# Kernel tuning notes

Measured on AMD Instinct MI355X. Metric: run time of the kernel, lower is better.

The kernel has to match this reference:

```python
import jax, jax.numpy as jnp
from jax import lax
import numpy as np

IMG = 2048.0            # square image size (W=H)
STRIDES = [32, 64, 128]
FEATS = [64, 32, 16]    # IMG / stride
NUM_CLASSES = 80
BATCH = 8
SCORE_THRESH = 0.2
NMS_THRESH = 0.6
TOPK = 1000             # topk_candidates per level
DETS = 100              # detections_per_img


def make_anchors(fs, stride):
    # square anchors of size==stride centered on the feature grid (AnchorGenerator with ratio 1.0)
    c = (jnp.arange(fs, dtype=jnp.float32) + 0.5) * stride
    cy, cx = jnp.meshgrid(c, c, indexing='ij')
    cx, cy = cx.reshape(-1), cy.reshape(-1)
    h = stride / 2.0
    return jnp.stack([cx - h, cy - h, cx + h, cy + h], axis=1)


def setup_inputs() -> dict:
    key = jax.random.key(0)
    inp = {}
    for i, (fs, s) in enumerate(zip(FEATS, STRIDES)):
        hw = fs * fs
        key, k1, k2, k3 = jax.random.split(key, 4)
        inp[f'cls{i}'] = jax.random.normal(k1, (BATCH, hw, NUM_CLASSES), jnp.float32)
        inp[f'reg{i}'] = jax.random.uniform(k2, (BATCH, hw, 4), jnp.float32)
        inp[f'ctr{i}'] = jax.random.normal(k3, (BATCH, hw), jnp.float32)
        inp[f'anc{i}'] = make_anchors(fs, float(s))
    return inp


def _decode(rel, boxes):
    # BoxLinearCoder.decode_single with normalize_by_size=True
    cx = 0.5 * (boxes[:, 0] + boxes[:, 2])
    cy = 0.5 * (boxes[:, 1] + boxes[:, 3])
    w = boxes[:, 2] - boxes[:, 0]
    h = boxes[:, 3] - boxes[:, 1]
    rel = rel * jnp.stack([w, h, w, h], axis=1)
    return jnp.stack([cx - rel[:, 0], cy - rel[:, 1], cx + rel[:, 2], cy + rel[:, 3]], axis=1)


def _iou(b):
    # torchvision box_iou on a single set of boxes [N,4] -> [N,N]
    area = (b[:, 2] - b[:, 0]) * (b[:, 3] - b[:, 1])
    lt = jnp.maximum(b[:, None, :2], b[None, :, :2])
    rb = jnp.minimum(b[:, None, 2:], b[None, :, 2:])
    wh = jnp.clip(rb - lt, 0.0)
    inter = wh[..., 0] * wh[..., 1]
    return inter / (area[:, None] + area[None, :] - inter)


def _greedy_keep(iou):
    # classic greedy NMS on score-sorted boxes: suppress j>i with iou>thresh if i kept
    n = iou.shape[0]
    idx = jnp.arange(n)
    def body(i, keep):
        supp = keep[i] & (iou[i] > NMS_THRESH) & (idx > i)
        return keep & ~supp
    return lax.fori_loop(0, n, body, jnp.ones((n,), bool))


def _per_image(cls_l, reg_l, ctr_l, anc_l):
    boxes, scores, labels = [], [], []
    for cls, reg, ctr, anc in zip(cls_l, reg_l, ctr_l, anc_l):
        hw, c = cls.shape
        # scores = sqrt(sigmoid(cls) * sigmoid(ctrness)) flattened over anchors*classes
        sc = jnp.sqrt(jax.nn.sigmoid(cls) * jax.nn.sigmoid(ctr)[:, None]).reshape(-1)
        sc = jnp.where(sc > SCORE_THRESH, sc, -1.0)  # score threshold as mask (static shapes)
        ts, ti = lax.top_k(sc, TOPK)                 # per-level top-k candidates
        aidx = ti // c
        lab = ti % c
        b = jnp.clip(_decode(reg[aidx], anc[aidx]), 0.0, IMG)  # decode + clip to image
        boxes.append(b); scores.append(ts); labels.append(lab)
    boxes = jnp.concatenate(boxes)    # [3*TOPK, 4]
    scores = jnp.concatenate(scores)  # [3*TOPK]
    labels = jnp.concatenate(labels)  # [3*TOPK]
    n = scores.shape[0]
    # batched_nms via per-class coordinate offsets
    off = labels.astype(boxes.dtype) * (IMG + 1.0)
    ss, oi = lax.top_k(scores, n)     # sort candidates by score desc
    bs = boxes[oi] + off[oi][:, None]
    keep = lax.stop_gradient(_greedy_keep(_iou(bs)))
    fsc = jnp.where(keep & (ss > 0), ss, -1.0)
    fs, fi = lax.top_k(fsc, DETS)     # keep detections_per_img; score==-1 marks padding
    return boxes[oi][fi], fs, labels[oi][fi]


def reference(cls0, cls1, cls2, reg0, reg1, reg2, ctr0, ctr1, ctr2, anc0, anc1, anc2):
    f = jax.vmap(lambda c0, c1, c2, r0, r1, r2, t0, t1, t2: _per_image(
        [c0, c1, c2], [r0, r1, r2], [t0, t1, t2], [anc0, anc1, anc2]))
    return f(cls0, cls1, cls2, reg0, reg1, reg2, ctr0, ctr1, ctr2)
```

## Files before the change

### kernel.cpp

```cpp
#include <hip/hip_runtime.h>

#define NCLS  80
#define SELK  256
#define NLVL  3
#define NIMG  8
#define DETS  100
#define CAP   512
#define NDEC  512
#define HBINS 4096
#define NHBLK 16
#define NCBLK 16
#define QBASE 0x3F800000u
#define QMAX  0x41C80000u
#define IMGSZ 2048.0f


__device__ __forceinline__ float sigm(float x) {
    if (x >= 0.f) return 1.f / (1.f + expf(-x));
    float e = expf(x);
    return e / (1.f + e);
}

__device__ __forceinline__ unsigned int qbits(float ea, float t1) {
    return __float_as_uint(__fmul_rn(__fadd_rn(1.f, ea), t1));
}

__device__ __forceinline__ void lvl_select(int level,
    const float* c0, const float* c1, const float* c2,
    const float* t0, const float* t1, const float* t2,
    const float** cls, const float** ctr, int* hw) {
    if (level == 0)      { *cls = c0; *ctr = t0; *hw = 4096; }
    else if (level == 1) { *cls = c1; *ctr = t1; *hw = 1024; }
    else                 { *cls = c2; *ctr = t2; *hw = 256; }
}


__global__ void k_hist(const float* c0, const float* c1, const float* c2,
                       const float* t0, const float* t1, const float* t2,
                       unsigned int* parts, unsigned int* counters) {
    int level = blockIdx.z, img = blockIdx.y;
    int pair = img * NLVL + level;
    if (blockIdx.x == 0 && threadIdx.x == 0) counters[pair * 16] = 0;
    const float* cls; const float* ctr; int hw;
    lvl_select(level, c0, c1, c2, t0, t1, t2, &cls, &ctr, &hw);
    int n4 = hw * (NCLS / 4);
    const float4* cl4 = (const float4*)(cls + (size_t)img * hw * NCLS);
    const float* ct = ctr + (size_t)img * hw;
    __shared__ unsigned int h[HBINS];
    for (int i = threadIdx.x; i < HBINS; i += 256) h[i] = 0;
    __syncthreads();
    for (int i = blockIdx.x * 256 + threadIdx.x; i < n4; i += NHBLK * 256) {
        float4 v = cl4[i];
        int a = i / (NCLS / 4);
        float eb = expf(-ct[a]);
        float t1 = __fadd_rn(1.f, eb);
        #pragma unroll
        for (int k = 0; k < 4; ++k) {
            float x = (k == 0) ? v.x : (k == 1) ? v.y : (k == 2) ? v.z : v.w;
            unsigned int qb = qbits(expf(-x), t1);
            if (qb < QMAX) {
                unsigned int bin = (qb - QBASE) >> 13;
                if (bin > HBINS - 1) bin = HBINS - 1;
                atomicAdd(&h[bin], 1u);
            }
        }
    }
    __syncthreads();
    unsigned int* P = parts + ((size_t)(pair * NHBLK + blockIdx.x)) * HBINS;
    for (int i = threadIdx.x; i < HBINS; i += 256) P[i] = h[i];
}


__global__ void k_collect(const float* c0, const float* c1, const float* c2,
                          const float* t0, const float* t1, const float* t2,
                          const unsigned int* parts, unsigned int* counters,
                          unsigned long long* buf) {
    int level = blockIdx.z, img = blockIdx.y;
    int pair = img * NLVL + level;
    int tid = threadIdx.x;
    __shared__ unsigned int hb[HBINS];
    __shared__ unsigned int segsum[256];
    __shared__ unsigned int pref[256];
    __shared__ unsigned long long sbuf[CAP];
    __shared__ unsigned int scnt, sbase, Vsh;
    if (tid == 0) scnt = 0;
    {
        unsigned int acc[HBINS / 256];
        #pragma unroll
        for (int j = 0; j < HBINS / 256; ++j) acc[j] = 0;
        for (int blk = 0; blk < NHBLK; ++blk) {
            const unsigned int* P = parts + ((size_t)(pair * NHBLK + blk)) * HBINS;
            #pragma unroll
            for (int j = 0; j < HBINS / 256; ++j) acc[j] += P[tid + 256 * j];
        }
        #pragma unroll
        for (int j = 0; j < HBINS / 256; ++j) hb[tid + 256 * j] = acc[j];
    }
    __syncthreads();
    {
        unsigned int seg = 0;
        #pragma unroll
        for (int j = 0; j < 16; ++j) seg += hb[16 * tid + j];
        segsum[tid] = seg;
        pref[tid] = seg;
        __syncthreads();
        for (int off = 1; off < 256; off <<= 1) {
            unsigned int v = (tid >= off) ? pref[tid - off] : 0u;
            __syncthreads();
            pref[tid] += v;
            __syncthreads();
        }
        unsigned int incl = pref[tid];
        unsigned int excl = incl - segsum[tid];
        if (excl < (unsigned int)SELK && incl >= (unsigned int)SELK) {
            unsigned int cum = excl; int B = HBINS - 1;
            for (int b = 16 * tid; b < 16 * tid + 16; ++b) {
                cum += hb[b];
                if (cum >= (unsigned int)SELK) { B = b; break; }
            }
            Vsh = (B >= HBINS - 1) ? QMAX : (QBASE + ((unsigned int)(B + 1) << 13));
        }
        if (tid == 255 && pref[255] < (unsigned int)SELK)
            Vsh = QMAX;
    }
    __syncthreads();
    unsigned int V = Vsh;

    const float* cls; const float* ctr; int hw;
    lvl_select(level, c0, c1, c2, t0, t1, t2, &cls, &ctr, &hw);
    int n4 = hw * (NCLS / 4);
    const float4* cl4 = (const float4*)(cls + (size_t)img * hw * NCLS);
    const float* ct = ctr + (size_t)img * hw;
    for (int i = blockIdx.x * 256 + tid; i < n4; i += NCBLK * 256) {
        float4 v = cl4[i];
        int a = i / (NCLS / 4);
        float cta = ct[a];
        float eb = expf(-cta);
        float t1 = __fadd_rn(1.f, eb);
        #pragma unroll
        for (int k = 0; k < 4; ++k) {
            float x = (k == 0) ? v.x : (k == 1) ? v.y : (k == 2) ? v.z : v.w;
            unsigned int qb = qbits(expf(-x), t1);
            if (qb < V) {
                float s = sqrtf(sigm(x) * sigm(cta));
                unsigned int e = (unsigned int)(4 * i + k);
                unsigned int p = ((unsigned int)level << 19) | e;
                unsigned int slot = atomicAdd(&scnt, 1u);
                if (slot < CAP)
                    sbuf[slot] = ((unsigned long long)__float_as_uint(s) << 32) | (~p);
            }
        }
    }
    __syncthreads();
    unsigned int cl_n = scnt; if (cl_n > CAP) cl_n = CAP;
    if (tid == 0)
        sbase = atomicAdd(&counters[pair * 16], cl_n);
    __syncthreads();
    unsigned int base = sbase;
    for (unsigned int idx = tid; idx < cl_n; idx += 256) {
        unsigned int g = base + idx;
        if (g < CAP) buf[(size_t)pair * CAP + g] = sbuf[idx];
    }
}


__global__ void __launch_bounds__(512)
k_merge_nms(const unsigned long long* buf, const unsigned int* counters,
            const float* r0, const float* r1, const float* r2,
            const float* a0, const float* a1, const float* a2,
            float* out) {
    int img = blockIdx.x;
    int tid = threadIdx.x;
    __shared__ unsigned long long S[3 * CAP];
    __shared__ unsigned long long Mbuf[2 * CAP];
    __shared__ float4 sbx[64]; __shared__ float sar[64];
    __shared__ float4 koff[DETS]; __shared__ float karr[DETS];
    __shared__ float4 kb[DETS]; __shared__ float ks[DETS]; __shared__ int kl[DETS];
    __shared__ float4 rb[DETS]; __shared__ int rl[DETS];
    float4* wbox = (float4*)Mbuf;
    int*    wlab = (int*)(S + CAP);

    for (int l = 0; l < NLVL; ++l) {
        int pair = img * NLVL + l;
        int c = (int)counters[pair * 16]; if (c > CAP) c = CAP;
        const unsigned long long* B = buf + (size_t)pair * CAP;
        S[l * CAP + tid] = (tid < c) ? B[tid] : 0ull;
    }
    __syncthreads();
    {
        volatile unsigned long long* vS = S;
        bool prev_cross = false;
        for (int k2 = 2; k2 <= CAP; k2 <<= 1) {
            for (int j = k2 >> 1; j > 0; j >>= 1) {
                bool cross = (j >= 64);
                if (cross || prev_cross) __syncthreads();
                int i = tid, ixj = i ^ j;
                if (ixj > i) {
                    bool up = ((i & k2) == 0);
                    #pragma unroll
                    for (int seg = 0; seg < NLVL; ++seg) {
                        int base = seg * CAP;
                        unsigned long long a = vS[base + i], b = vS[base + ixj];
                        if (up ? (a < b) : (a > b)) { vS[base + i] = b; vS[base + ixj] = a; }
                    }
                }
                prev_cross = cross;
            }
        }
    }
    __syncthreads();
    for (int k = tid; k < 2 * CAP; k += 512) {
        int lo = max(0, k - CAP), hi = min(k, CAP);
        while (lo < hi) {
            int mid = (lo + hi) >> 1;
            if (S[mid] > S[CAP + (k - mid - 1)]) lo = mid + 1; else hi = mid;
        }
        int i = lo, j = k - lo;
        unsigned long long av = (i < CAP) ? S[i] : 0ull;
        unsigned long long bv = (j < CAP) ? S[CAP + j] : 0ull;
        Mbuf[k] = (av > bv) ? av : bv;
    }
    __syncthreads();
    {
        int k = tid;
        int lo = max(0, k - CAP), hi = k;
        while (lo < hi) {
            int mid = (lo + hi) >> 1;
            if (Mbuf[mid] > S[2 * CAP + (k - mid - 1)]) lo = mid + 1; else hi = mid;
        }
        int i = lo, j = k - lo;
        unsigned long long mv = (i < 2 * CAP) ? Mbuf[i] : 0ull;
        unsigned long long cv = (j < CAP) ? S[2 * CAP + j] : 0ull;
        unsigned long long rk = (mv > cv) ? mv : cv;
        __syncthreads();
        S[k] = rk;
    }
    __syncthreads();
    {
        unsigned long long key = S[tid];
        float4 b4 = make_float4(0.f, 0.f, 0.f, 0.f); int lbv = 0;
        if (key != 0ull) {
            unsigned int p = (~((unsigned int)key)) & 0x1FFFFFu;
            int lvl = (int)(p >> 19);
            unsigned int e = p & 0x7FFFFu;
            int a = (int)(e / NCLS); lbv = (int)(e % NCLS);
            const float* anc; const float* reg; int hw;
            if (lvl == 0)      { anc = a0; reg = r0; hw = 4096; }
            else if (lvl == 1) { anc = a1; reg = r1; hw = 1024; }
            else               { anc = a2; reg = r2; hw = 256; }
            const float* rg = reg + (size_t)img * hw * 4;
            float ax1 = anc[a * 4 + 0], ay1 = anc[a * 4 + 1];
            float ax2 = anc[a * 4 + 2], ay2 = anc[a * 4 + 3];
            float cx = 0.5f * (ax1 + ax2), cy = 0.5f * (ay1 + ay2);
            float w = ax2 - ax1, h = ay2 - ay1;
            float e0 = rg[a * 4 + 0] * w, e1 = rg[a * 4 + 1] * h;
            float e2 = rg[a * 4 + 2] * w, e3 = rg[a * 4 + 3] * h;
            b4.x = fminf(fmaxf(cx - e0, 0.f), IMGSZ);
            b4.y = fminf(fmaxf(cy - e1, 0.f), IMGSZ);
            b4.z = fminf(fmaxf(cx + e2, 0.f), IMGSZ);
            b4.w = fminf(fmaxf(cy + e3, 0.f), IMGSZ);
        }
        wbox[tid] = b4; wlab[tid] = lbv;
    }
    __syncthreads();

    if (tid >= 64) return;
    int lane = tid;
    unsigned long long lmask_lt = (lane == 0) ? 0ull : (~0ull >> (64 - lane));

    int kept = 0, ring = 0, r = 0;

    while (kept < DETS && r < NDEC) {
        int rank = r + lane;
        unsigned long long key = (rank < NDEC) ? S[rank] : 0ull;
        unsigned int bits = (unsigned int)(key >> 32);
        unsigned long long pm = __ballot(bits != 0u);
        int npos = (pm == ~0ull) ? 64 : (int)__builtin_ctzll(~pm);
        if (npos == 0) break;

        float4 bx = make_float4(0.f, 0.f, 0.f, 0.f); int lb = 0;
        if (lane < npos) { bx = wbox[rank]; lb = wlab[rank]; }
        float off = (float)lb * (IMGSZ + 1.0f);
        float ox1 = bx.x + off, oy1 = bx.y + off;
        float ox2 = bx.z + off, oy2 = bx.w + off;
        float car = (ox2 - ox1) * (oy2 - oy1);
        sbx[lane] = make_float4(ox1, oy1, ox2, oy2);
        sar[lane] = car;

        bool supk = false;
        for (int k2 = 0; k2 < kept; ++k2) {
            float4 kk = koff[k2]; float ka = karr[k2];
            float lx = fmaxf(kk.x, ox1), ly = fmaxf(kk.y, oy1);
            float rx = fminf(kk.z, ox2), ry = fminf(kk.w, oy2);
            float w = fmaxf(rx - lx, 0.f), h = fmaxf(ry - ly, 0.f);
            float inter = w * h;
            supk = supk || (inter / (ka + car - inter) > 0.6f);
        }
        unsigned long long col = 0ull;
        for (int i = 0; i < npos; ++i) {
            float4 c = sbx[i]; float ca = sar[i];
            float lx = fmaxf(c.x, ox1), ly = fmaxf(c.y, oy1);
            float rx = fminf(c.z, ox2), ry = fminf(c.w, oy2);
            float w = fmaxf(rx - lx, 0.f), h = fmaxf(ry - ly, 0.f);
            float inter = w * h;
            if ((inter / (ca + car - inter) > 0.6f) && (i < lane)) col |= (1ull << i);
        }
        unsigned long long undecided = __ballot((lane < npos) && !supk);
        unsigned long long aliveSel = 0ull;
        int capleft = DETS - kept;
        int lastSlot = npos - 1;
        while (undecided) {
            int i = (int)__builtin_ctzll(undecided);
            aliveSel |= (1ull << i);
            undecided &= ~(1ull << i);
            if (--capleft == 0) { lastSlot = i; break; }
            unsigned long long row = __ballot(((col >> i) & 1ull) != 0ull);
            undecided &= ~row;
        }
        unsigned long long region = (lastSlot >= 63) ? ~0ull : ((1ull << (lastSlot + 1)) - 1ull);
        region &= (npos >= 64) ? ~0ull : ((1ull << npos) - 1ull);
        unsigned long long rejm = region & ~aliveSel;

        if ((aliveSel >> lane) & 1ull) {
            int ki = kept + (int)__popcll(aliveSel & lmask_lt);
            koff[ki] = make_float4(ox1, oy1, ox2, oy2); karr[ki] = car;
            kb[ki] = bx; ks[ki] = __uint_as_float(bits); kl[ki] = lb;
        }
        if ((rejm >> lane) & 1ull) {
            int ri = ring + (int)__popcll(rejm & lmask_lt);
            if (ri < DETS) { rb[ri] = bx; rl[ri] = lb; }
        }
        kept += (int)__popcll(aliveSel);
        ring += (int)__popcll(rejm);
        r += lastSlot + 1;
    }

    while (kept < DETS && ring < DETS && r < NDEC) {
        int rank = r + lane;
        if (rank < NDEC) {
            int ri = ring + lane;
            if (ri < DETS) { rb[ri] = wbox[rank]; rl[ri] = wlab[rank]; }
        }
        int take = NDEC - r; if (take > 64) take = 64;
        ring += take;
        r += 64;
    }

    for (int k = lane; k < DETS; k += 64) {
        float4 bxo; float scv; int lv;
        if (k < kept) { bxo = kb[k]; scv = ks[k]; lv = kl[k]; }
        else { int q = k - kept; bxo = rb[q]; scv = -1.0f; lv = rl[q]; }
        float* ob = out + ((size_t)img * DETS + k) * 4;
        ob[0] = bxo.x; ob[1] = bxo.y; ob[2] = bxo.z; ob[3] = bxo.w;
        out[NIMG * DETS * 4 + img * DETS + k] = scv;
        out[NIMG * DETS * 5 + img * DETS + k] = (float)lv;
    }
}


extern "C" void kernel_launch(void* const* d_in, const int* in_sizes, int n_in,
                              void* d_out, int out_size, void* d_ws, size_t ws_size,
                              hipStream_t stream) {
    (void)in_sizes; (void)n_in; (void)out_size; (void)ws_size;
    const float* cls0 = (const float*)d_in[0];
    const float* reg0 = (const float*)d_in[1];
    const float* ctr0 = (const float*)d_in[2];
    const float* anc0 = (const float*)d_in[3];
    const float* cls1 = (const float*)d_in[4];
    const float* reg1 = (const float*)d_in[5];
    const float* ctr1 = (const float*)d_in[6];
    const float* anc1 = (const float*)d_in[7];
    const float* cls2 = (const float*)d_in[8];
    const float* reg2 = (const float*)d_in[9];
    const float* ctr2 = (const float*)d_in[10];
    const float* anc2 = (const float*)d_in[11];
    float* out = (float*)d_out;
    char* ws = (char*)d_ws;

    const size_t OFF_PARTS = 0;
    const size_t OFF_CNT   = 6291456;
    const size_t OFF_BUF   = 6292992;

    unsigned int* parts = (unsigned int*)(ws + OFF_PARTS);
    unsigned int* cnt   = (unsigned int*)(ws + OFF_CNT);
    unsigned long long* buf = (unsigned long long*)(ws + OFF_BUF);

    k_hist<<<dim3(NHBLK, NIMG, NLVL), 256, 0, stream>>>(
        cls0, cls1, cls2, ctr0, ctr1, ctr2, parts, cnt);
    k_collect<<<dim3(NCBLK, NIMG, NLVL), 256, 0, stream>>>(
        cls0, cls1, cls2, ctr0, ctr1, ctr2, parts, cnt, buf);
    k_merge_nms<<<NIMG, 512, 0, stream>>>(buf, cnt, reg0, reg1, reg2,
                                          anc0, anc1, anc2, out);
}
```

Baseline: 180.0 us.

## Register-shuffle sort and block-parallel IoU bitmask precompute for NMS

The per-level shared-memory bitonic sort is replaced by a 64-wide register sort using wave shuffles, followed by merge-path passes that ping-pong between two shared buffers. For the top 256 ranked candidates, all 512 threads now precompute an upper-triangular IoU suppression bitmask in parallel. The single-wave greedy loop then resolves suppression with mask ANDs against the kept bits instead of recomputing IoUs serially. This adds shared memory and assumes candidate windows stay 64-aligned in the fast path, falling back to the old per-box IoU path beyond rank 256.

```diff
diff --git a/kernel.cpp b/kernel.cpp
--- a/kernel.cpp
+++ b/kernel.cpp
@@ -7,6 +7,7 @@
 #define DETS  100
 #define CAP   512
 #define NDEC  512
+#define NMSW  256
 #define HBINS 4096
 #define NHBLK 16
 #define NCBLK 16
@@ -23,6 +24,14 @@
 
 __device__ __forceinline__ unsigned int qbits(float ea, float t1) {
     return __float_as_uint(__fmul_rn(__fadd_rn(1.f, ea), t1));
+}
+
+__device__ __forceinline__ unsigned long long shfl_u64(unsigned long long v, int lane) {
+    int lo = (int)(unsigned int)v;
+    int hi = (int)(unsigned int)(v >> 32);
+    lo = __shfl(lo, lane, 64);
+    hi = __shfl(hi, lane, 64);
+    return ((unsigned long long)(unsigned int)hi << 32) | (unsigned int)lo;
 }
 
 __device__ __forceinline__ void lvl_select(int level,
@@ -171,54 +180,81 @@
             float* out) {
     int img = blockIdx.x;
     int tid = threadIdx.x;
+    int lane = tid & 63;
     __shared__ unsigned long long S[3 * CAP];
-    __shared__ unsigned long long Mbuf[2 * CAP];
+    __shared__ unsigned long long T[3 * CAP];
+    __shared__ float4 wbox[NDEC];
+    __shared__ int    wlab[NDEC];
+    __shared__ float4 obx[NMSW];
+    __shared__ float  oar[NMSW];
+    __shared__ unsigned long long colmask[NMSW][4];
     __shared__ float4 sbx[64]; __shared__ float sar[64];
     __shared__ float4 koff[DETS]; __shared__ float karr[DETS];
     __shared__ float4 kb[DETS]; __shared__ float ks[DETS]; __shared__ int kl[DETS];
     __shared__ float4 rb[DETS]; __shared__ int rl[DETS];
-    float4* wbox = (float4*)Mbuf;
-    int*    wlab = (int*)(S + CAP);
-
-    for (int l = 0; l < NLVL; ++l) {
-        int pair = img * NLVL + l;
-        int c = (int)counters[pair * 16]; if (c > CAP) c = CAP;
-        const unsigned long long* B = buf + (size_t)pair * CAP;
-        S[l * CAP + tid] = (tid < c) ? B[tid] : 0ull;
-    }
-    __syncthreads();
-    {
-        volatile unsigned long long* vS = S;
-        bool prev_cross = false;
-        for (int k2 = 2; k2 <= CAP; k2 <<= 1) {
-            for (int j = k2 >> 1; j > 0; j >>= 1) {
-                bool cross = (j >= 64);
-                if (cross || prev_cross) __syncthreads();
-                int i = tid, ixj = i ^ j;
-                if (ixj > i) {
-                    bool up = ((i & k2) == 0);
-                    #pragma unroll
-                    for (int seg = 0; seg < NLVL; ++seg) {
-                        int base = seg * CAP;
-                        unsigned long long a = vS[base + i], b = vS[base + ixj];
-                        if (up ? (a < b) : (a > b)) { vS[base + i] = b; vS[base + ixj] = a; }
-                    }
+
+    unsigned long long v0, v1, v2;
+    {
+        int c0n = (int)counters[(img * NLVL + 0) * 16]; if (c0n > CAP) c0n = CAP;
+        int c1n = (int)counters[(img * NLVL + 1) * 16]; if (c1n > CAP) c1n = CAP;
+        int c2n = (int)counters[(img * NLVL + 2) * 16]; if (c2n > CAP) c2n = CAP;
+        v0 = (tid < c0n) ? buf[(size_t)(img * NLVL + 0) * CAP + tid] : 0ull;
+        v1 = (tid < c1n) ? buf[(size_t)(img * NLVL + 1) * CAP + tid] : 0ull;
+        v2 = (tid < c2n) ? buf[(size_t)(img * NLVL + 2) * CAP + tid] : 0ull;
+    }
+    #pragma unroll
+    for (int k = 2; k <= 64; k <<= 1) {
+        #pragma unroll
+        for (int j = k >> 1; j > 0; j >>= 1) {
+            unsigned long long p0 = shfl_u64(v0, lane ^ j);
+            unsigned long long p1 = shfl_u64(v1, lane ^ j);
+            unsigned long long p2 = shfl_u64(v2, lane ^ j);
+            bool up = ((lane & k) == 0);
+            bool lower = ((lane & j) == 0);
+            bool mx = (up == lower);
+            v0 = mx ? (v0 > p0 ? v0 : p0) : (v0 < p0 ? v0 : p0);
+            v1 = mx ? (v1 > p1 ? v1 : p1) : (v1 < p1 ? v1 : p1);
+            v2 = mx ? (v2 > p2 ? v2 : p2) : (v2 < p2 ? v2 : p2);
+        }
+    }
+    S[0 * CAP + tid] = v0;
+    S[1 * CAP + tid] = v1;
+    S[2 * CAP + tid] = v2;
+    __syncthreads();
+
+    {
+        unsigned long long* src = S;
+        unsigned long long* dst = T;
+        for (int m = 64; m <= 256; m <<= 1) {
+            for (int o = tid; o < 3 * CAP; o += 512) {
+                int seg = o >> 9, k = o & (CAP - 1);
+                int pw = 2 * m;
+                int ab = seg * CAP + (k / pw) * pw;
+                int q = k % pw;
+                int lo = max(0, q - m), hi = min(q, m);
+                while (lo < hi) {
+                    int mid = (lo + hi) >> 1;
+                    if (src[ab + mid] > src[ab + m + (q - mid - 1)]) lo = mid + 1; else hi = mid;
                 }
-                prev_cross = cross;
-            }
-        }
-    }
-    __syncthreads();
+                int i2 = lo, j2 = q - lo;
+                unsigned long long av = (i2 < m) ? src[ab + i2] : 0ull;
+                unsigned long long bv = (j2 < m) ? src[ab + m + j2] : 0ull;
+                dst[o] = (av > bv) ? av : bv;
+            }
+            __syncthreads();
+            unsigned long long* tmp = src; src = dst; dst = tmp;
+        }
+    }
     for (int k = tid; k < 2 * CAP; k += 512) {
         int lo = max(0, k - CAP), hi = min(k, CAP);
         while (lo < hi) {
             int mid = (lo + hi) >> 1;
-            if (S[mid] > S[CAP + (k - mid - 1)]) lo = mid + 1; else hi = mid;
+            if (T[mid] > T[CAP + (k - mid - 1)]) lo = mid + 1; else hi = mid;
         }
         int i = lo, j = k - lo;
-        unsigned long long av = (i < CAP) ? S[i] : 0ull;
-        unsigned long long bv = (j < CAP) ? S[CAP + j] : 0ull;
-        Mbuf[k] = (av > bv) ? av : bv;
+        unsigned long long av = (i < CAP) ? T[i] : 0ull;
+        unsigned long long bv = (j < CAP) ? T[CAP + j] : 0ull;
+        S[k] = (av > bv) ? av : bv;
     }
     __syncthreads();
     {
@@ -226,16 +262,17 @@
         int lo = max(0, k - CAP), hi = k;
         while (lo < hi) {
             int mid = (lo + hi) >> 1;
-            if (Mbuf[mid] > S[2 * CAP + (k - mid - 1)]) lo = mid + 1; else hi = mid;
+            if (S[mid] > T[2 * CAP + (k - mid - 1)]) lo = mid + 1; else hi = mid;
         }
         int i = lo, j = k - lo;
-        unsigned long long mv = (i < 2 * CAP) ? Mbuf[i] : 0ull;
-        unsigned long long cv = (j < CAP) ? S[2 * CAP + j] : 0ull;
+        unsigned long long mv = (i < 2 * CAP) ? S[i] : 0ull;
+        unsigned long long cv = (j < CAP) ? T[2 * CAP + j] : 0ull;
         unsigned long long rk = (mv > cv) ? mv : cv;
         __syncthreads();
         S[k] = rk;
     }
     __syncthreads();
+
     {
         unsigned long long key = S[tid];
         float4 b4 = make_float4(0.f, 0.f, 0.f, 0.f); int lbv = 0;
@@ -264,9 +301,39 @@
     }
     __syncthreads();
 
+    if (tid < NMSW) {
+        float4 bx = wbox[tid]; int lb = wlab[tid];
+        float off = (float)lb * (IMGSZ + 1.0f);
+        float ox1 = bx.x + off, oy1 = bx.y + off;
+        float ox2 = bx.z + off, oy2 = bx.w + off;
+        obx[tid] = make_float4(ox1, oy1, ox2, oy2);
+        oar[tid] = (ox2 - ox1) * (oy2 - oy1);
+    }
+    __syncthreads();
+    for (int Tk = tid; Tk < NMSW * 4; Tk += 512) {
+        int j = Tk & (NMSW - 1);
+        int w = Tk >> 8;
+        float4 oj = obx[j]; float aj = oar[j];
+        unsigned long long m = 0ull;
+        int base = w * 64;
+        for (int jj = 0; jj < 64; ++jj) {
+            int i = base + jj;
+            if (i < j) {
+                float4 oi = obx[i]; float ai = oar[i];
+                float lx = fmaxf(oi.x, oj.x), ly = fmaxf(oi.y, oj.y);
+                float rx = fminf(oi.z, oj.z), ry = fminf(oi.w, oj.w);
+                float ww = fmaxf(rx - lx, 0.f), hh = fmaxf(ry - ly, 0.f);
+                float inter = ww * hh;
+                if (inter / (ai + aj - inter) > 0.6f) m |= (1ull << jj);
+            }
+        }
+        colmask[j][w] = m;
+    }
+    __syncthreads();
+
     if (tid >= 64) return;
-    int lane = tid;
     unsigned long long lmask_lt = (lane == 0) ? 0ull : (~0ull >> (64 - lane));
+    unsigned long long K[4] = {0ull, 0ull, 0ull, 0ull};
 
     int kept = 0, ring = 0, r = 0;
 
@@ -284,26 +351,39 @@
         float ox1 = bx.x + off, oy1 = bx.y + off;
         float ox2 = bx.z + off, oy2 = bx.w + off;
         float car = (ox2 - ox1) * (oy2 - oy1);
-        sbx[lane] = make_float4(ox1, oy1, ox2, oy2);
-        sar[lane] = car;
 
         bool supk = false;
-        for (int k2 = 0; k2 < kept; ++k2) {
-            float4 kk = koff[k2]; float ka = karr[k2];
-            float lx = fmaxf(kk.x, ox1), ly = fmaxf(kk.y, oy1);
-            float rx = fminf(kk.z, ox2), ry = fminf(kk.w, oy2);
-            float w = fmaxf(rx - lx, 0.f), h = fmaxf(ry - ly, 0.f);
-            float inter = w * h;
-            supk = supk || (inter / (ka + car - inter) > 0.6f);
-        }
         unsigned long long col = 0ull;
-        for (int i = 0; i < npos; ++i) {
-            float4 c = sbx[i]; float ca = sar[i];
-            float lx = fmaxf(c.x, ox1), ly = fmaxf(c.y, oy1);
-            float rx = fminf(c.z, ox2), ry = fminf(c.w, oy2);
-            float w = fmaxf(rx - lx, 0.f), h = fmaxf(ry - ly, 0.f);
-            float inter = w * h;
-            if ((inter / (ca + car - inter) > 0.6f) && (i < lane)) col |= (1ull << i);
+        if (r < NMSW) {
+            int b = r >> 6;
+            int i = rank;
+            unsigned long long cm0 = colmask[i][0], cm1 = colmask[i][1];
+            unsigned long long cm2 = colmask[i][2], cm3 = colmask[i][3];
+            unsigned long long sup = 0ull;
+            if (b > 0) sup |= cm0 & K[0];
+            if (b > 1) sup |= cm1 & K[1];
+            if (b > 2) sup |= cm2 & K[2];
+            supk = sup != 0ull;
+            col = (b == 0) ? cm0 : (b == 1) ? cm1 : (b == 2) ? cm2 : cm3;
+        } else {
+            sbx[lane] = make_float4(ox1, oy1, ox2, oy2);
+            sar[lane] = car;
+            for (int k2 = 0; k2 < kept; ++k2) {
+                float4 kk = koff[k2]; float ka = karr[k2];
+                float lx = fmaxf(kk.x, ox1), ly = fmaxf(kk.y, oy1);
+                float rx = fminf(kk.z, ox2), ry = fminf(kk.w, oy2);
+                float w = fmaxf(rx - lx, 0.f), h = fmaxf(ry - ly, 0.f);
+                float inter = w * h;
+                supk = supk || (inter / (ka + car - inter) > 0.6f);
+            }
+            for (int i = 0; i < npos; ++i) {
+                float4 c = sbx[i]; float ca = sar[i];
+                float lx = fmaxf(c.x, ox1), ly = fmaxf(c.y, oy1);
+                float rx = fminf(c.z, ox2), ry = fminf(c.w, oy2);
+                float w = fmaxf(rx - lx, 0.f), h = fmaxf(ry - ly, 0.f);
+                float inter = w * h;
+                if ((inter / (ca + car - inter) > 0.6f) && (i < lane)) col |= (1ull << i);
+            }
         }
         unsigned long long undecided = __ballot((lane < npos) && !supk);
         unsigned long long aliveSel = 0ull;
@@ -320,6 +400,8 @@
         unsigned long long region = (lastSlot >= 63) ? ~0ull : ((1ull << (lastSlot + 1)) - 1ull);
         region &= (npos >= 64) ? ~0ull : ((1ull << npos) - 1ull);
         unsigned long long rejm = region & ~aliveSel;
+
+        if (r < NMSW) K[r >> 6] = aliveSel;
 
         if ((aliveSel >> lane) & 1ull) {
             int ki = kept + (int)__popcll(aliveSel & lmask_lt);
```

Result: faster. 163.1 us (-9.4%).
